# Performance work log

Measured on AMD Instinct MI355X. Metric: run time of the kernel, lower is better.

## Reference

```python
import jax, jax.numpy as jnp
import numpy as np
from jax import lax

D_MODEL, D_STATE, D_CONV, EXPAND = 1024, 16, 4, 2
D_INNER = EXPAND * D_MODEL
B_SZ, L_SEQ = 2, 2048

# BitLinear quantization (BitNet b1.58 style, STE via stop_gradient)

def _weight_quant(w):
    scale = jnp.maximum(jnp.mean(jnp.abs(w)), 1e-5)
    q = jnp.clip(jnp.round(w / scale), -1.0, 1.0) * scale
    return w + lax.stop_gradient(q - w)

def _act_quant(x):
    s = 127.0 / jnp.maximum(jnp.max(jnp.abs(x), axis=-1, keepdims=True), 1e-5)
    q = jnp.clip(jnp.round(x * s), -128.0, 127.0) / s
    return x + lax.stop_gradient(q - x)

def bitlinear(x, w, b=None):
    y = _act_quant(x) @ _weight_quant(w).T
    return y + b if b is not None else y


def setup_inputs() -> dict:
    key = jax.random.key(0)
    ks = jax.random.split(key, 9)
    inp = {
        "x": jax.random.normal(ks[0], (B_SZ, L_SEQ, D_MODEL), jnp.float32),
        "in_proj_w": jax.random.normal(ks[1], (2 * D_INNER, D_MODEL), jnp.float32) * 0.02,
        "conv_w": jax.random.normal(ks[2], (D_INNER, 1, D_CONV), jnp.float32) * 0.2,
        "conv_b": jnp.zeros((D_INNER,), jnp.float32),
        "delta_w": jax.random.normal(ks[3], (D_STATE, D_INNER), jnp.float32) * 0.02,
        "delta_b": jnp.zeros((D_STATE,), jnp.float32),
        "B_w": jax.random.normal(ks[4], (D_STATE, D_INNER), jnp.float32) * 0.02,
        "C_w": jax.random.normal(ks[5], (D_STATE, D_INNER), jnp.float32) * 0.02,
        "out_w": jax.random.normal(ks[6], (D_MODEL, D_INNER), jnp.float32) * 0.02,
        "D": jnp.ones((D_INNER,), jnp.float32),
        "log_A": -0.5 * jnp.log(1.0 + jnp.arange(1, D_STATE + 1, dtype=jnp.float32) / D_STATE),
    }
    return inp


def reference(x, in_proj_w, conv_w, conv_b, delta_w, delta_b, B_w, C_w, out_w, D, log_A):
    B, L, _ = x.shape
    # input projection + SiLU gating
    xp = bitlinear(x, in_proj_w)                      # [B, L, 2*d_inner]
    x_gate, x_input = jnp.split(xp, 2, axis=-1)
    x_input = jax.nn.silu(x_gate) * x_input          # [B, L, d_inner]
    # causal depthwise conv1d (padding d_conv-1 then truncation == left-pad)
    xc = lax.conv_general_dilated(
        x_input.transpose(0, 2, 1), conv_w, window_strides=(1,),
        padding=[(D_CONV - 1, 0)], feature_group_count=D_INNER)
    x_input = (xc + conv_b[None, :, None]).transpose(0, 2, 1)  # [B, L, d_inner]
    # selective parameters
    delta = bitlinear(x_input, delta_w, delta_b)     # [B, L, N]
    A_d = jnp.exp(delta * log_A[None, None, :])      # [B, L, N]
    B_mat = bitlinear(x_input, B_w)                  # [B, L, N]
    C_mat = bitlinear(x_input, C_w)                  # [B, L, N]
    # diagonal state recurrence via lax.scan over time
    dB = delta * B_mat                               # [B, L, N]
    def step(h, ins):
        a_t, db_t, c_t = ins                         # each [B, N]
        h = a_t * h + db_t
        return h, jnp.sum(c_t * h, axis=-1)          # signal: [B]
    h0 = jnp.zeros((B, D_STATE), x.dtype)
    _, sig = lax.scan(step, h0, (A_d.transpose(1, 0, 2), dB.transpose(1, 0, 2), C_mat.transpose(1, 0, 2)))
    state_signal = sig.T[:, :, None]                 # [B, L, 1]
    y_inner = x_input * (jax.nn.sigmoid(state_signal) + D[None, None, :])
    return bitlinear(y_inner, out_w)                 # [B, L, d_model]
```

## Files before the change

### kernel.cpp

```cpp
#include <hip/hip_runtime.h>
#include <hip/hip_bf16.h>

typedef signed char i8;
typedef int v4i __attribute__((ext_vector_type(4)));

#define LSTR 80
#define MFMA_I8 __builtin_amdgcn_mfma_i32_16x16x64_i8

__device__ __forceinline__ void gld16(const void* g, void* l) {
  __builtin_amdgcn_global_load_lds(
      (const __attribute__((address_space(1))) unsigned int*)g,
      (__attribute__((address_space(3))) unsigned int*)l, 16, 0, 0);
}

#define LADDR(rr, c) ((((rr) >> 1) << 7) + (((rr) & 1) << 6) + ((((c) ^ (((rr) >> 1) & 3))) << 4))

__global__ __launch_bounds__(256) void k_abssum_all(const float* __restrict__ w0, const float* __restrict__ w1,
                                                    const float* __restrict__ w2, const float* __restrict__ w3,
                                                    const float* __restrict__ w4, double* __restrict__ partial) {
  int b = blockIdx.x;
  const float* w; int n, nb, bg;
  if (b < 256)      { w = w0; n = 4194304; nb = 256; bg = b; }
  else if (b < 272) { w = w1; n = 32768;   nb = 16;  bg = b - 256; }
  else if (b < 288) { w = w2; n = 32768;   nb = 16;  bg = b - 272; }
  else if (b < 304) { w = w3; n = 32768;   nb = 16;  bg = b - 288; }
  else              { w = w4; n = 2097152; nb = 128; bg = b - 304; }
  __shared__ double sd[256];
  double acc = 0.0;
  for (int i = bg * 256 + threadIdx.x; i < n; i += nb * 256) acc += (double)fabsf(w[i]);
  sd[threadIdx.x] = acc;
  __syncthreads();
  for (int s = 128; s > 0; s >>= 1) {
    if (threadIdx.x < s) sd[threadIdx.x] += sd[threadIdx.x + s];
    __syncthreads();
  }
  if (threadIdx.x == 0) partial[b] = sd[0];
}

__global__ void k_finalize(const double* __restrict__ partial, float* __restrict__ scales) {
  int m = threadIdx.x;
  if (m >= 5) return;
  const int off[6] = {0, 256, 272, 288, 304, 432};
  const double cnt[5] = {4194304.0, 32768.0, 32768.0, 32768.0, 2097152.0};
  double s = 0.0;
  for (int i = off[m]; i < off[m + 1]; ++i) s += partial[i];
  scales[m] = fmaxf((float)(s / cnt[m]), 1e-5f);
}

__global__ __launch_bounds__(256) void k_wquant_all(const float* __restrict__ w0, const float* __restrict__ w1,
                                                    const float* __restrict__ w2, const float* __restrict__ w3,
                                                    const float* __restrict__ w4, const float* __restrict__ scales,
                                                    i8* __restrict__ tin, i8* __restrict__ t2, i8* __restrict__ tout) {
  int b = blockIdx.x;
  const float* w; i8* t; int m, n;
  if (b < 4096)      { w = w0; t = tin;          m = 0; n = 4194304; }
  else if (b < 4128) { w = w1; t = t2;           m = 1; n = 32768; b -= 4096; }
  else if (b < 4160) { w = w2; t = t2 + 32768;   m = 2; n = 32768; b -= 4128; }
  else if (b < 4192) { w = w3; t = t2 + 65536;   m = 3; n = 32768; b -= 4160; }
  else               { w = w4; t = tout;         m = 4; n = 2097152; b -= 4192; }
  int idx = (b * 256 + threadIdx.x) * 4;
  if (idx >= n) return;
  float scale = scales[m];
  float4 v = *(const float4*)(w + idx);
  char4 q;
  q.x = (i8)fminf(fmaxf(rintf(v.x / scale), -1.f), 1.f);
  q.y = (i8)fminf(fmaxf(rintf(v.y / scale), -1.f), 1.f);
  q.z = (i8)fminf(fmaxf(rintf(v.z / scale), -1.f), 1.f);
  q.w = (i8)fminf(fmaxf(rintf(v.w / scale), -1.f), 1.f);
  *(char4*)(t + idx) = q;
}

template <int W>
__global__ __launch_bounds__(256) void k_actquant(const float* __restrict__ x,
                                                  i8* __restrict__ q, float* __restrict__ srow) {
  constexpr int E = W / 256;
  const int r = blockIdx.x, tid = threadIdx.x;
  const float* xr = x + (size_t)r * W;
  float v[E];
  float m = 0.f;
#pragma unroll
  for (int j = 0; j < E; j += 4) {
    float4 t = *(const float4*)(xr + tid * E + j);
    v[j] = t.x; v[j + 1] = t.y; v[j + 2] = t.z; v[j + 3] = t.w;
    m = fmaxf(m, fmaxf(fmaxf(fabsf(t.x), fabsf(t.y)), fmaxf(fabsf(t.z), fabsf(t.w))));
  }
  __shared__ float sm[4];
  __shared__ float sbc;
#pragma unroll
  for (int off = 32; off > 0; off >>= 1) m = fmaxf(m, __shfl_xor(m, off));
  if ((tid & 63) == 0) sm[tid >> 6] = m;
  __syncthreads();
  if (tid == 0) {
    float mm = fmaxf(fmaxf(sm[0], sm[1]), fmaxf(sm[2], sm[3]));
    float s = 127.0f / fmaxf(mm, 1e-5f);
    sbc = s;
    srow[r] = s;
  }
  __syncthreads();
  float s = sbc;
#pragma unroll
  for (int j = 0; j < E; j += 4) {
    char4 c;
    c.x = (i8)fminf(fmaxf(rintf(v[j] * s), -128.f), 127.f);
    c.y = (i8)fminf(fmaxf(rintf(v[j + 1] * s), -128.f), 127.f);
    c.z = (i8)fminf(fmaxf(rintf(v[j + 2] * s), -128.f), 127.f);
    c.w = (i8)fminf(fmaxf(rintf(v[j + 3] * s), -128.f), 127.f);
    *(char4*)(q + (size_t)r * W + tid * E + j) = c;
  }
}

__global__ __launch_bounds__(256) void k_gemm1(const i8* __restrict__ qx, const i8* __restrict__ tin,
                                               const float* __restrict__ sx, const float* __restrict__ scales,
                                               float* __restrict__ gated) {
  __shared__ i8 A_[2][8192], G_[2][4096], V_[2][4096];
  __shared__ float frow[128];
  const int tid = threadIdx.x;
  const int r0 = blockIdx.x * 128, c0 = blockIdx.y * 64;
  if (tid < 128) frow[tid] = scales[0] / sx[r0 + tid];
  const int lane = tid & 63, wv = tid >> 6;
  const int wm = wv >> 1, wn = wv & 1;
  const int lo = lane & 15, hi = lane >> 4;
  const int sr0 = ((tid >> 3) << 1) | ((tid >> 2) & 1);
  const int sc0 = ((tid & 3) ^ ((tid >> 3) & 3)) << 4;
  const i8* gA0 = qx + (size_t)(r0 + sr0) * 1024 + sc0;
  const i8* gA1 = qx + (size_t)(r0 + 64 + sr0) * 1024 + sc0;
  const i8* gG  = tin + (size_t)(c0 + sr0) * 1024 + sc0;
  const i8* gV  = tin + (size_t)(2048 + c0 + sr0) * 1024 + sc0;
  const int ldsb = wv << 10;
  v4i accg[4][2], accv[4][2];
#pragma unroll
  for (int m = 0; m < 4; ++m)
#pragma unroll
    for (int n = 0; n < 2; ++n) {
      accg[m][n] = (v4i){0, 0, 0, 0};
      accv[m][n] = (v4i){0, 0, 0, 0};
    }

#define STAGE1(t, bi)                              \
  {                                                \
    const int kb = (t) << 6;                       \
    gld16(gA0 + kb, A_[bi] + ldsb);                \
    gld16(gA1 + kb, A_[bi] + 4096 + ldsb);         \
    gld16(gG + kb, G_[bi] + ldsb);                 \
    gld16(gV + kb, V_[bi] + ldsb);                 \
  }

#define COMPUTE1(bi)                                                                       \
  {                                                                                        \
    v4i a[4];                                                                              \
    _Pragma("unroll") for (int m = 0; m < 4; ++m)                                          \
        a[m] = *(const v4i*)&A_[bi][LADDR(wm * 64 + m * 16 + lo, hi)];                     \
    v4i bg0 = *(const v4i*)&G_[bi][LADDR(wn * 32 + lo, hi)];                               \
    v4i bg1 = *(const v4i*)&G_[bi][LADDR(wn * 32 + 16 + lo, hi)];                          \
    v4i bv0 = *(const v4i*)&V_[bi][LADDR(wn * 32 + lo, hi)];                               \
    v4i bv1 = *(const v4i*)&V_[bi][LADDR(wn * 32 + 16 + lo, hi)];                          \
    __builtin_amdgcn_s_setprio(1);                                                         \
    _Pragma("unroll") for (int m = 0; m < 4; ++m) {                                        \
      accg[m][0] = MFMA_I8(a[m], bg0, accg[m][0], 0, 0, 0);                                \
      accg[m][1] = MFMA_I8(a[m], bg1, accg[m][1], 0, 0, 0);                                \
      accv[m][0] = MFMA_I8(a[m], bv0, accv[m][0], 0, 0, 0);                                \
      accv[m][1] = MFMA_I8(a[m], bv1, accv[m][1], 0, 0, 0);                                \
    }                                                                                      \
    __builtin_amdgcn_s_setprio(0);                                                         \
  }

  STAGE1(0, 0);
  asm volatile("s_waitcnt vmcnt(0)" ::: "memory");
  __builtin_amdgcn_s_barrier();
#pragma unroll
  for (int t = 0; t < 16; ++t) {
    const int bi = t & 1;
    if (t + 1 < 16) STAGE1(t + 1, bi ^ 1);
    COMPUTE1(bi);
    asm volatile("s_waitcnt vmcnt(0)" ::: "memory");
    __builtin_amdgcn_s_barrier();
  }
#undef STAGE1
#undef COMPUTE1

#pragma unroll
  for (int m = 0; m < 4; ++m)
#pragma unroll
    for (int n = 0; n < 2; ++n)
#pragma unroll
      for (int rg = 0; rg < 4; ++rg) {
        int row = wm * 64 + m * 16 + hi * 4 + rg;
        int col = wn * 32 + n * 16 + lo;
        float f = frow[row];
        float g = (float)accg[m][n][rg] * f;
        float v = (float)accv[m][n][rg] * f;
        float sg = 1.0f / (1.0f + expf(-g));
        gated[(size_t)(r0 + row) * 2048 + c0 + col] = g * sg * v;
      }
}

__global__ __launch_bounds__(256) void k_convq(const float* __restrict__ g, const float* __restrict__ cw,
                                               const float* __restrict__ cb, float* __restrict__ xo,
                                               i8* __restrict__ q, float* __restrict__ srow) {
  const int tid = threadIdx.x;
  const int r0 = blockIdx.x * 8;
  const int l0 = r0 & 2047;
  const int ch = tid * 8;
  const int lane = tid & 63, wv = tid >> 6;
  float wt[4][8];
#pragma unroll
  for (int j = 0; j < 8; ++j) {
    float4 w = *(const float4*)(cw + (ch + j) * 4);
    wt[0][j] = w.x; wt[1][j] = w.y; wt[2][j] = w.z; wt[3][j] = w.w;
  }
  float bias[8];
  {
    float4 b0 = *(const float4*)(cb + ch), b1 = *(const float4*)(cb + ch + 4);
    bias[0] = b0.x; bias[1] = b0.y; bias[2] = b0.z; bias[3] = b0.w;
    bias[4] = b1.x; bias[5] = b1.y; bias[6] = b1.z; bias[7] = b1.w;
  }
  const float* gb = g + (size_t)r0 * 2048 + ch;
  float wm3[8], wm2[8], wm1[8];
  if (l0 != 0) {
    float4 a, b;
    a = *(const float4*)(gb - 3 * 2048); b = *(const float4*)(gb - 3 * 2048 + 4);
    wm3[0]=a.x; wm3[1]=a.y; wm3[2]=a.z; wm3[3]=a.w; wm3[4]=b.x; wm3[5]=b.y; wm3[6]=b.z; wm3[7]=b.w;
    a = *(const float4*)(gb - 2 * 2048); b = *(const float4*)(gb - 2 * 2048 + 4);
    wm2[0]=a.x; wm2[1]=a.y; wm2[2]=a.z; wm2[3]=a.w; wm2[4]=b.x; wm2[5]=b.y; wm2[6]=b.z; wm2[7]=b.w;
    a = *(const float4*)(gb - 1 * 2048); b = *(const float4*)(gb - 1 * 2048 + 4);
    wm1[0]=a.x; wm1[1]=a.y; wm1[2]=a.z; wm1[3]=a.w; wm1[4]=b.x; wm1[5]=b.y; wm1[6]=b.z; wm1[7]=b.w;
  } else {
#pragma unroll
    for (int j = 0; j < 8; ++j) { wm3[j] = 0.f; wm2[j] = 0.f; wm1[j] = 0.f; }
  }
  float* xop = xo + (size_t)r0 * 2048 + ch;
  float y[8][8];
  float rowmax[8];
#pragma unroll
  for (int l = 0; l < 8; ++l) {
    float cur[8];
    {
      float4 a = *(const float4*)(gb + l * 2048), b = *(const float4*)(gb + l * 2048 + 4);
      cur[0]=a.x; cur[1]=a.y; cur[2]=a.z; cur[3]=a.w; cur[4]=b.x; cur[5]=b.y; cur[6]=b.z; cur[7]=b.w;
    }
    float m = 0.f;
#pragma unroll
    for (int j = 0; j < 8; ++j) {
      float v = bias[j];
      v = fmaf(wt[0][j], wm3[j], v);
      v = fmaf(wt[1][j], wm2[j], v);
      v = fmaf(wt[2][j], wm1[j], v);
      v = fmaf(wt[3][j], cur[j], v);
      y[l][j] = v;
      m = fmaxf(m, fabsf(v));
    }
    rowmax[l] = m;
    *(float4*)(xop + l * 2048) = make_float4(y[l][0], y[l][1], y[l][2], y[l][3]);
    *(float4*)(xop + l * 2048 + 4) = make_float4(y[l][4], y[l][5], y[l][6], y[l][7]);
#pragma unroll
    for (int j = 0; j < 8; ++j) { wm3[j] = wm2[j]; wm2[j] = wm1[j]; wm1[j] = cur[j]; }
  }
  __shared__ float sred[8][4];
  __shared__ float sscale[8];
#pragma unroll
  for (int l = 0; l < 8; ++l) {
    float m = rowmax[l];
#pragma unroll
    for (int off = 32; off > 0; off >>= 1) m = fmaxf(m, __shfl_xor(m, off));
    if (lane == 0) sred[l][wv] = m;
  }
  __syncthreads();
  if (tid < 8) {
    float mm = fmaxf(fmaxf(sred[tid][0], sred[tid][1]), fmaxf(sred[tid][2], sred[tid][3]));
    float s = 127.0f / fmaxf(mm, 1e-5f);
    sscale[tid] = s;
    srow[r0 + tid] = s;
  }
  __syncthreads();
  i8* qp = q + (size_t)r0 * 2048 + ch;
#pragma unroll
  for (int l = 0; l < 8; ++l) {
    float s = sscale[l];
    char4 c0q, c1q;
    c0q.x = (i8)fminf(fmaxf(rintf(y[l][0] * s), -128.f), 127.f);
    c0q.y = (i8)fminf(fmaxf(rintf(y[l][1] * s), -128.f), 127.f);
    c0q.z = (i8)fminf(fmaxf(rintf(y[l][2] * s), -128.f), 127.f);
    c0q.w = (i8)fminf(fmaxf(rintf(y[l][3] * s), -128.f), 127.f);
    c1q.x = (i8)fminf(fmaxf(rintf(y[l][4] * s), -128.f), 127.f);
    c1q.y = (i8)fminf(fmaxf(rintf(y[l][5] * s), -128.f), 127.f);
    c1q.z = (i8)fminf(fmaxf(rintf(y[l][6] * s), -128.f), 127.f);
    c1q.w = (i8)fminf(fmaxf(rintf(y[l][7] * s), -128.f), 127.f);
    *(char4*)(qp + l * 2048) = c0q;
    *(char4*)(qp + l * 2048 + 4) = c1q;
  }
}

__global__ __launch_bounds__(256) void k_gemm2(const i8* __restrict__ q2, const i8* __restrict__ t2,
                                               int* __restrict__ ipart) {
  __shared__ i8 As[64 * LSTR];
  __shared__ i8 Bs[48 * LSTR];
  const int tid = threadIdx.x;
  const int r0 = blockIdx.x * 64;
  const int kb = blockIdx.y * 1024;
  const int lrow = tid >> 2, lk = (tid & 3) * 16;
  const int lane = tid & 63, wv = tid >> 6;
  const int fr = lane & 15, fk = (lane >> 4) * 16;
  v4i acc[3];
#pragma unroll
  for (int s = 0; s < 3; ++s) acc[s] = (v4i){0, 0, 0, 0};
  for (int ks = 0; ks < 16; ++ks) {
    const int k0 = kb + ks * 64;
    __syncthreads();
    *(v4i*)&As[lrow * LSTR + lk] = *(const v4i*)&q2[(size_t)(r0 + lrow) * 2048 + k0 + lk];
    if (tid < 192)
      *(v4i*)&Bs[(tid >> 2) * LSTR + (tid & 3) * 16] = *(const v4i*)&t2[(size_t)(tid >> 2) * 2048 + k0 + (tid & 3) * 16];
    __syncthreads();
    v4i a = *(const v4i*)&As[(wv * 16 + fr) * LSTR + fk];
#pragma unroll
    for (int s = 0; s < 3; ++s) {
      v4i b = *(const v4i*)&Bs[(s * 16 + fr) * LSTR + fk];
      acc[s] = MFMA_I8(a, b, acc[s], 0, 0, 0);
    }
  }
#pragma unroll
  for (int s = 0; s < 3; ++s)
#pragma unroll
    for (int rg = 0; rg < 4; ++rg) {
      int row = wv * 16 + (lane >> 4) * 4 + rg;
      int col = s * 16 + (lane & 15);
      ipart[(size_t)blockIdx.y * 196608 + (size_t)(r0 + row) * 48 + col] = acc[s][rg];
    }
}

__global__ __launch_bounds__(256) void k_xform(const int* __restrict__ ip, const float* __restrict__ s2,
                                               const float* __restrict__ scales, const float* __restrict__ dbias,
                                               const float* __restrict__ logA, float* __restrict__ At,
                                               float* __restrict__ dBt, float* __restrict__ Ct) {
  int idx = blockIdx.x * 256 + threadIdx.x;
  int r = idx >> 4, n = idx & 15;
  int b = r >> 11, l = r & 2047;
  float fr = 1.0f / s2[r];
  int base = r * 48;
  float dd = (float)(ip[base + n] + ip[196608 + base + n]) * (scales[1] * fr) + dbias[n];
  float Bv = (float)(ip[base + 16 + n] + ip[196608 + base + 16 + n]) * (scales[2] * fr);
  float Cv = (float)(ip[base + 32 + n] + ip[196608 + base + 32 + n]) * (scales[3] * fr);
  int o = ((b * 16 + n) << 11) | l;
  At[o] = expf(dd * logA[n]);
  dBt[o] = dd * Bv;
  Ct[o] = Cv;
}

__global__ __launch_bounds__(256) void k_scan(const float* __restrict__ At, const float* __restrict__ dBt,
                                              const float* __restrict__ Ct, float* __restrict__ ch) {
  const int i = threadIdx.x;
  const int base = blockIdx.x << 11;
  float a[8], db[8], c[8];
  {
    const float4* p = (const float4*)(At + base + i * 8);
    float4 t0 = p[0], t1 = p[1];
    a[0]=t0.x; a[1]=t0.y; a[2]=t0.z; a[3]=t0.w; a[4]=t1.x; a[5]=t1.y; a[6]=t1.z; a[7]=t1.w;
  }
  {
    const float4* p = (const float4*)(dBt + base + i * 8);
    float4 t0 = p[0], t1 = p[1];
    db[0]=t0.x; db[1]=t0.y; db[2]=t0.z; db[3]=t0.w; db[4]=t1.x; db[5]=t1.y; db[6]=t1.z; db[7]=t1.w;
  }
  {
    const float4* p = (const float4*)(Ct + base + i * 8);
    float4 t0 = p[0], t1 = p[1];
    c[0]=t0.x; c[1]=t0.y; c[2]=t0.z; c[3]=t0.w; c[4]=t1.x; c[5]=t1.y; c[6]=t1.z; c[7]=t1.w;
  }
  float Ac = 1.f, Bc = 0.f;
#pragma unroll
  for (int j = 0; j < 8; ++j) { Bc = a[j] * Bc + db[j]; Ac *= a[j]; }
  __shared__ float sA[256], sB[256];
  sA[i] = Ac; sB[i] = Bc;
  __syncthreads();
  for (int off = 1; off < 256; off <<= 1) {
    float pA = 1.f, pB = 0.f;
    if (i >= off) { pA = sA[i - off]; pB = sB[i - off]; }
    __syncthreads();
    Bc = Ac * pB + Bc;
    Ac = Ac * pA;
    sA[i] = Ac; sB[i] = Bc;
    __syncthreads();
  }
  float h = (i > 0) ? sB[i - 1] : 0.f;
  float o[8];
#pragma unroll
  for (int j = 0; j < 8; ++j) { h = a[j] * h + db[j]; o[j] = c[j] * h; }
  float4* po = (float4*)(ch + base + i * 8);
  po[0] = make_float4(o[0], o[1], o[2], o[3]);
  po[1] = make_float4(o[4], o[5], o[6], o[7]);
}

__global__ __launch_bounds__(256) void k_yq(const float* __restrict__ xin, const float* __restrict__ chb,
                                            const float* __restrict__ Dp, i8* __restrict__ q,
                                            float* __restrict__ srow) {
  const int tid = threadIdx.x;
  const int r0 = blockIdx.x * 8;
  const int b = r0 >> 11, l0 = r0 & 2047;
  const int lane = tid & 63, wv = tid >> 6;
  __shared__ float ssig[8 * 16];
  __shared__ float ssg[8];
  __shared__ float sred[8][4];
  __shared__ float sscale[8];
  if (tid < 128) {
    int n = tid >> 3, li = tid & 7;
    ssig[li * 16 + n] = chb[((size_t)(b * 16 + n) << 11) | (l0 + li)];
  }
  __syncthreads();
  if (tid < 8) {
    float s = 0.f;
    for (int n = 0; n < 16; ++n) s += ssig[tid * 16 + n];
    ssg[tid] = 1.0f / (1.0f + expf(-s));
  }
  __syncthreads();
  const int ch = tid * 8;
  float dreg[8];
  {
    float4 d0 = *(const float4*)(Dp + ch), d1 = *(const float4*)(Dp + ch + 4);
    dreg[0]=d0.x; dreg[1]=d0.y; dreg[2]=d0.z; dreg[3]=d0.w;
    dreg[4]=d1.x; dreg[5]=d1.y; dreg[6]=d1.z; dreg[7]=d1.w;
  }
  const float* xr = xin + (size_t)r0 * 2048 + ch;
  float y[8][8];
  float rowmax[8];
#pragma unroll
  for (int l = 0; l < 8; ++l) {
    float sg = ssg[l];
    float4 a = *(const float4*)(xr + l * 2048);
    float4 c = *(const float4*)(xr + l * 2048 + 4);
    y[l][0] = a.x * (sg + dreg[0]);
    y[l][1] = a.y * (sg + dreg[1]);
    y[l][2] = a.z * (sg + dreg[2]);
    y[l][3] = a.w * (sg + dreg[3]);
    y[l][4] = c.x * (sg + dreg[4]);
    y[l][5] = c.y * (sg + dreg[5]);
    y[l][6] = c.z * (sg + dreg[6]);
    y[l][7] = c.w * (sg + dreg[7]);
    float m = 0.f;
#pragma unroll
    for (int j = 0; j < 8; ++j) m = fmaxf(m, fabsf(y[l][j]));
    rowmax[l] = m;
  }
#pragma unroll
  for (int l = 0; l < 8; ++l) {
    float m = rowmax[l];
#pragma unroll
    for (int off = 32; off > 0; off >>= 1) m = fmaxf(m, __shfl_xor(m, off));
    if (lane == 0) sred[l][wv] = m;
  }
  __syncthreads();
  if (tid < 8) {
    float mm = fmaxf(fmaxf(sred[tid][0], sred[tid][1]), fmaxf(sred[tid][2], sred[tid][3]));
    float s = 127.0f / fmaxf(mm, 1e-5f);
    sscale[tid] = s;
    srow[r0 + tid] = s;
  }
  __syncthreads();
  i8* qp = q + (size_t)r0 * 2048 + ch;
#pragma unroll
  for (int l = 0; l < 8; ++l) {
    float s = sscale[l];
    char4 c0q, c1q;
    c0q.x = (i8)fminf(fmaxf(rintf(y[l][0] * s), -128.f), 127.f);
    c0q.y = (i8)fminf(fmaxf(rintf(y[l][1] * s), -128.f), 127.f);
    c0q.z = (i8)fminf(fmaxf(rintf(y[l][2] * s), -128.f), 127.f);
    c0q.w = (i8)fminf(fmaxf(rintf(y[l][3] * s), -128.f), 127.f);
    c1q.x = (i8)fminf(fmaxf(rintf(y[l][4] * s), -128.f), 127.f);
    c1q.y = (i8)fminf(fmaxf(rintf(y[l][5] * s), -128.f), 127.f);
    c1q.z = (i8)fminf(fmaxf(rintf(y[l][6] * s), -128.f), 127.f);
    c1q.w = (i8)fminf(fmaxf(rintf(y[l][7] * s), -128.f), 127.f);
    *(char4*)(qp + l * 2048) = c0q;
    *(char4*)(qp + l * 2048 + 4) = c1q;
  }
}

__global__ __launch_bounds__(512) void k_gemm3(const i8* __restrict__ q3, const i8* __restrict__ tout,
                                               const float* __restrict__ s3, const float* __restrict__ scales,
                                               float* __restrict__ out) {
  __shared__ i8 A_[2][8192], B_[2][8192];
  __shared__ float frow[128];
  const int tid = threadIdx.x;
  const int r0 = blockIdx.x * 128, c0 = blockIdx.y * 128;
  if (tid < 128) frow[tid] = scales[4] / s3[r0 + tid];
  const int lane = tid & 63, wv = tid >> 6;
  const int wm = wv >> 1, wn = wv & 1;
  const int lo = lane & 15, hi = lane >> 4;
  const int d0 = tid << 4;
  const int sr0 = ((d0 >> 7) << 1) | ((d0 >> 6) & 1);
  const int sc0 = ((((d0 >> 4) & 3) ^ ((sr0 >> 1) & 3)) << 4);
  const i8* gA = q3 + (size_t)(r0 + sr0) * 2048 + sc0;
  const i8* gB = tout + (size_t)(c0 + sr0) * 2048 + sc0;
  const int ldsb = wv << 10;
  v4i acc[2][4];
#pragma unroll
  for (int m = 0; m < 2; ++m)
#pragma unroll
    for (int n = 0; n < 4; ++n) acc[m][n] = (v4i){0, 0, 0, 0};

#define STAGE3(t, bi)                       \
  {                                         \
    const int kb = (t) << 6;                \
    gld16(gA + kb, A_[bi] + ldsb);          \
    gld16(gB + kb, B_[bi] + ldsb);          \
  }

  STAGE3(0, 0);
  for (int t = 0; t < 32; ++t) {
    const int bi = t & 1;
    if (t < 31) {
      STAGE3(t + 1, bi ^ 1);
      asm volatile("s_waitcnt vmcnt(2)" ::: "memory");
    } else {
      asm volatile("s_waitcnt vmcnt(0)" ::: "memory");
    }
    __builtin_amdgcn_s_barrier();
    v4i a[2];
#pragma unroll
    for (int m = 0; m < 2; ++m) a[m] = *(const v4i*)&A_[bi][LADDR(wm * 32 + m * 16 + lo, hi)];
    v4i b0 = *(const v4i*)&B_[bi][LADDR(wn * 64 + lo, hi)];
    v4i b1 = *(const v4i*)&B_[bi][LADDR(wn * 64 + 16 + lo, hi)];
    __builtin_amdgcn_s_barrier();
    __builtin_amdgcn_s_setprio(1);
#pragma unroll
    for (int m = 0; m < 2; ++m) {
      acc[m][0] = MFMA_I8(a[m], b0, acc[m][0], 0, 0, 0);
      acc[m][1] = MFMA_I8(a[m], b1, acc[m][1], 0, 0, 0);
    }
    __builtin_amdgcn_s_setprio(0);
    __builtin_amdgcn_s_barrier();
    b0 = *(const v4i*)&B_[bi][LADDR(wn * 64 + 32 + lo, hi)];
    b1 = *(const v4i*)&B_[bi][LADDR(wn * 64 + 48 + lo, hi)];
    __builtin_amdgcn_s_barrier();
    __builtin_amdgcn_s_setprio(1);
#pragma unroll
    for (int m = 0; m < 2; ++m) {
      acc[m][2] = MFMA_I8(a[m], b0, acc[m][2], 0, 0, 0);
      acc[m][3] = MFMA_I8(a[m], b1, acc[m][3], 0, 0, 0);
    }
    __builtin_amdgcn_s_setprio(0);
    __builtin_amdgcn_s_barrier();
  }
#undef STAGE3

#pragma unroll
  for (int m = 0; m < 2; ++m)
#pragma unroll
    for (int n = 0; n < 4; ++n)
#pragma unroll
      for (int rg = 0; rg < 4; ++rg) {
        int row = wm * 32 + m * 16 + hi * 4 + rg;
        int col = wn * 64 + n * 16 + lo;
        out[(size_t)(r0 + row) * 1024 + c0 + col] = (float)acc[m][n][rg] * frow[row];
      }
}

extern "C" void kernel_launch(void* const* d_in, const int* in_sizes, int n_in,
                              void* d_out, int out_size, void* d_ws, size_t ws_size,
                              hipStream_t stream) {
  const float* x     = (const float*)d_in[0];
  const float* win   = (const float*)d_in[1];
  const float* cw    = (const float*)d_in[2];
  const float* cb    = (const float*)d_in[3];
  const float* dw    = (const float*)d_in[4];
  const float* dbias = (const float*)d_in[5];
  const float* bw    = (const float*)d_in[6];
  const float* cmw   = (const float*)d_in[7];
  const float* ow    = (const float*)d_in[8];
  const float* Dp    = (const float*)d_in[9];
  const float* logA  = (const float*)d_in[10];
  float* out = (float*)d_out;

  char* p = (char*)d_ws;
  float* gated = (float*)p;   p += (size_t)4096 * 2048 * 4;
  float* xin   = (float*)p;   p += (size_t)4096 * 2048 * 4;
  char* qx_rgn = p;           p += (size_t)4096 * 1024;
  char* tin_rgn = p;          p += (size_t)2 * 2048 * 1024;
  i8* tout = (i8*)p;          p += (size_t)1024 * 2048;
  i8* t2   = (i8*)p;          p += (size_t)48 * 2048;
  i8* q2   = (i8*)p;          p += (size_t)4096 * 2048;
  i8* q3   = (i8*)p;          p += (size_t)4096 * 2048;
  float* sx  = (float*)p;     p += (size_t)4096 * 4;
  float* s2  = (float*)p;     p += (size_t)4096 * 4;
  float* s3  = (float*)p;     p += (size_t)4096 * 4;
  float* scales = (float*)p;  p += 256;
  double* partial = (double*)p;

  i8* qx  = (i8*)qx_rgn;
  i8* tin = (i8*)tin_rgn;
  int* ipart = (int*)qx_rgn;
  float* At  = (float*)tin_rgn;
  float* dBt = At + 65536;
  float* Ct  = dBt + 65536;
  float* chb = Ct + 65536;

  k_abssum_all<<<432, 256, 0, stream>>>(win, dw, bw, cmw, ow, partial);
  k_finalize<<<1, 64, 0, stream>>>(partial, scales);
  k_wquant_all<<<6240, 256, 0, stream>>>(win, dw, bw, cmw, ow, scales, tin, t2, tout);

  k_actquant<1024><<<4096, 256, 0, stream>>>(x, qx, sx);
  k_gemm1<<<dim3(32, 32), 256, 0, stream>>>(qx, tin, sx, scales, gated);
  k_convq<<<512, 256, 0, stream>>>(gated, cw, cb, xin, q2, s2);
  k_gemm2<<<dim3(64, 2), 256, 0, stream>>>(q2, t2, ipart);
  k_xform<<<256, 256, 0, stream>>>(ipart, s2, scales, dbias, logA, At, dBt, Ct);
  k_scan<<<32, 256, 0, stream>>>(At, dBt, Ct, chb);
  k_yq<<<512, 256, 0, stream>>>(xin, chb, Dp, q3, s3);
  k_gemm3<<<dim3(32, 8), 512, 0, stream>>>(q3, tout, s3, scales, out);
}
```

Before: 152.7 us.

## Give each wave private LDS buffers in gemm1 and drop block barriers

```diff
diff --git a/kernel.cpp b/kernel.cpp
--- a/kernel.cpp
+++ b/kernel.cpp
@@ -112,86 +112,87 @@
 __global__ __launch_bounds__(256) void k_gemm1(const i8* __restrict__ qx, const i8* __restrict__ tin,
                                                const float* __restrict__ sx, const float* __restrict__ scales,
                                                float* __restrict__ gated) {
-  __shared__ i8 A_[2][8192], G_[2][4096], V_[2][4096];
-  __shared__ float frow[128];
+  __shared__ i8 W_[4][2][10240];
   const int tid = threadIdx.x;
   const int r0 = blockIdx.x * 128, c0 = blockIdx.y * 64;
-  if (tid < 128) frow[tid] = scales[0] / sx[r0 + tid];
   const int lane = tid & 63, wv = tid >> 6;
-  const int wm = wv >> 1, wn = wv & 1;
   const int lo = lane & 15, hi = lane >> 4;
-  const int sr0 = ((tid >> 3) << 1) | ((tid >> 2) & 1);
-  const int sc0 = ((tid & 3) ^ ((tid >> 3) & 3)) << 4;
-  const i8* gA0 = qx + (size_t)(r0 + sr0) * 1024 + sc0;
-  const i8* gA1 = qx + (size_t)(r0 + 64 + sr0) * 1024 + sc0;
-  const i8* gG  = tin + (size_t)(c0 + sr0) * 1024 + sc0;
-  const i8* gV  = tin + (size_t)(2048 + c0 + sr0) * 1024 + sc0;
-  const int ldsb = wv << 10;
-  v4i accg[4][2], accv[4][2];
-#pragma unroll
-  for (int m = 0; m < 4; ++m)
-#pragma unroll
-    for (int n = 0; n < 2; ++n) {
+  const int srow = 2 * (lane >> 3) + ((lane >> 2) & 1);
+  const int schk = ((lane & 3) ^ ((lane >> 3) & 3)) << 4;
+  const i8* gA = qx + (size_t)(r0 + wv * 32 + srow) * 1024 + schk;
+  const i8* gG = tin + (size_t)(c0 + srow) * 1024 + schk;
+  const i8* gV = tin + (size_t)(2048 + c0 + srow) * 1024 + schk;
+  v4i accg[2][4], accv[2][4];
+#pragma unroll
+  for (int m = 0; m < 2; ++m)
+#pragma unroll
+    for (int n = 0; n < 4; ++n) {
       accg[m][n] = (v4i){0, 0, 0, 0};
       accv[m][n] = (v4i){0, 0, 0, 0};
     }
 
-#define STAGE1(t, bi)                              \
-  {                                                \
-    const int kb = (t) << 6;                       \
-    gld16(gA0 + kb, A_[bi] + ldsb);                \
-    gld16(gA1 + kb, A_[bi] + 4096 + ldsb);         \
-    gld16(gG + kb, G_[bi] + ldsb);                 \
-    gld16(gV + kb, V_[bi] + ldsb);                 \
-  }
-
-#define COMPUTE1(bi)                                                                       \
+#define STAGE1(t, s)                                        \
+  {                                                         \
+    const int kb = (t) << 6;                                \
+    i8* P = &W_[wv][s][0];                                  \
+    gld16(gA + kb, P);                                      \
+    gld16(gA + 16384 + kb, P + 1024);                       \
+    _Pragma("unroll") for (int i = 0; i < 4; ++i) {         \
+      gld16(gG + i * 16384 + kb, P + 2048 + i * 1024);      \
+      gld16(gV + i * 16384 + kb, P + 6144 + i * 1024);      \
+    }                                                       \
+  }
+
+#define COMPUTE1(s)                                                                        \
   {                                                                                        \
-    v4i a[4];                                                                              \
-    _Pragma("unroll") for (int m = 0; m < 4; ++m)                                          \
-        a[m] = *(const v4i*)&A_[bi][LADDR(wm * 64 + m * 16 + lo, hi)];                     \
-    v4i bg0 = *(const v4i*)&G_[bi][LADDR(wn * 32 + lo, hi)];                               \
-    v4i bg1 = *(const v4i*)&G_[bi][LADDR(wn * 32 + 16 + lo, hi)];                          \
-    v4i bv0 = *(const v4i*)&V_[bi][LADDR(wn * 32 + lo, hi)];                               \
-    v4i bv1 = *(const v4i*)&V_[bi][LADDR(wn * 32 + 16 + lo, hi)];                          \
+    const i8* P = &W_[wv][s][0];                                                           \
+    v4i a[2], bg[4], bv[4];                                                                \
+    _Pragma("unroll") for (int m = 0; m < 2; ++m)                                          \
+        a[m] = *(const v4i*)&P[LADDR(m * 16 + lo, hi)];                                    \
+    _Pragma("unroll") for (int n = 0; n < 4; ++n) {                                        \
+      bg[n] = *(const v4i*)&P[2048 + LADDR(n * 16 + lo, hi)];                              \
+      bv[n] = *(const v4i*)&P[6144 + LADDR(n * 16 + lo, hi)];                              \
+    }                                                                                      \
     __builtin_amdgcn_s_setprio(1);                                                         \
-    _Pragma("unroll") for (int m = 0; m < 4; ++m) {                                        \
-      accg[m][0] = MFMA_I8(a[m], bg0, accg[m][0], 0, 0, 0);                                \
-      accg[m][1] = MFMA_I8(a[m], bg1, accg[m][1], 0, 0, 0);                                \
-      accv[m][0] = MFMA_I8(a[m], bv0, accv[m][0], 0, 0, 0);                                \
-      accv[m][1] = MFMA_I8(a[m], bv1, accv[m][1], 0, 0, 0);                                \
+    _Pragma("unroll") for (int n = 0; n < 4; ++n)                                          \
+        _Pragma("unroll") for (int m = 0; m < 2; ++m) {                                    \
+      accg[m][n] = MFMA_I8(a[m], bg[n], accg[m][n], 0, 0, 0);                              \
+      accv[m][n] = MFMA_I8(a[m], bv[n], accv[m][n], 0, 0, 0);                              \
     }                                                                                      \
     __builtin_amdgcn_s_setprio(0);                                                         \
   }
 
   STAGE1(0, 0);
-  asm volatile("s_waitcnt vmcnt(0)" ::: "memory");
-  __builtin_amdgcn_s_barrier();
+  STAGE1(1, 1);
 #pragma unroll
   for (int t = 0; t < 16; ++t) {
-    const int bi = t & 1;
-    if (t + 1 < 16) STAGE1(t + 1, bi ^ 1);
-    COMPUTE1(bi);
-    asm volatile("s_waitcnt vmcnt(0)" ::: "memory");
-    __builtin_amdgcn_s_barrier();
+    if (t < 15) {
+      asm volatile("s_waitcnt vmcnt(10)" ::: "memory");
+    } else {
+      asm volatile("s_waitcnt vmcnt(0)" ::: "memory");
+    }
+    COMPUTE1(t & 1);
+    if (t + 2 < 16) STAGE1(t + 2, t & 1);
   }
 #undef STAGE1
 #undef COMPUTE1
 
-#pragma unroll
-  for (int m = 0; m < 4; ++m)
-#pragma unroll
-    for (int n = 0; n < 2; ++n)
-#pragma unroll
-      for (int rg = 0; rg < 4; ++rg) {
-        int row = wm * 64 + m * 16 + hi * 4 + rg;
-        int col = wn * 32 + n * 16 + lo;
-        float f = frow[row];
+  const float sc0 = scales[0];
+#pragma unroll
+  for (int m = 0; m < 2; ++m)
+#pragma unroll
+    for (int rg = 0; rg < 4; ++rg) {
+      int row = wv * 32 + m * 16 + hi * 4 + rg;
+      float f = sc0 / sx[r0 + row];
+#pragma unroll
+      for (int n = 0; n < 4; ++n) {
+        int col = n * 16 + lo;
         float g = (float)accg[m][n][rg] * f;
         float v = (float)accv[m][n][rg] * f;
         float sg = 1.0f / (1.0f + expf(-g));
         gated[(size_t)(r0 + row) * 2048 + c0 + col] = g * sg * v;
       }
+    }
 }
 
 __global__ __launch_bounds__(256) void k_convq(const float* __restrict__ g, const float* __restrict__ cw,
```

Result: slower. 157.0 us (+2.8%).
